# Kernel tuning notes

Hardware: AMD Instinct MI355X
Metric: run time of the kernel (lower is better)

Reference implementation:

```python
import jax, jax.numpy as jnp
import numpy as np

B, IN, H = 4096, 1024, 2048

def setup_inputs() -> dict:
    key = jax.random.key(0)
    ks = jax.random.split(key, 7)
    sk = (1.0 / H) ** 0.5
    return {
        "x": jax.random.normal(ks[0], (B, IN), dtype=jnp.float32),
        "prev_h": jax.random.normal(ks[1], (B, H), dtype=jnp.float32),
        "prev_c": jax.random.normal(ks[2], (B, H), dtype=jnp.float32),
        "W_i": jax.random.uniform(ks[3], (H, H + IN), dtype=jnp.float32, minval=-sk, maxval=sk),
        "W_f": jax.random.uniform(ks[4], (H, H + IN), dtype=jnp.float32, minval=-sk, maxval=sk),
        "W_o": jax.random.uniform(ks[5], (H, H + IN), dtype=jnp.float32, minval=-sk, maxval=sk),
        "W_c": jax.random.uniform(ks[6], (H, H + IN), dtype=jnp.float32, minval=-sk, maxval=sk),
    }

def reference(x, prev_h, prev_c, W_i, W_f, W_o, W_c):
    # concat (h, x) along features: [B, H+IN]
    hx = jnp.concatenate([prev_h, x], axis=1)
    # stack 4 gate weights -> single GEMM: [B, H+IN] @ [H+IN, 4H]
    W = jnp.concatenate([W_i, W_f, W_o, W_c], axis=0)  # [4H, H+IN]
    gates = hx @ W.T  # [B, 4H]
    gi, gf, go, gc = jnp.split(gates, 4, axis=1)
    i = jax.nn.sigmoid(gi)
    f = jax.nn.sigmoid(gf)
    o = jax.nn.sigmoid(go)
    c_tilde = jnp.tanh(gc)
    next_c = f * prev_c + i * c_tilde
    next_h = o * jnp.tanh(next_c)
    return next_h, next_c
```

## Files before the change

kernel.cpp:

```cpp
#include <hip/hip_runtime.h>
#include <hip/hip_bf16.h>


#define BATCH 4096
#define INW   1024
#define HID   2048
#define GK    3072
#define GN    8192

typedef __attribute__((ext_vector_type(8))) short short8;
typedef __attribute__((ext_vector_type(4))) float floatx4;

__device__ __forceinline__ unsigned short f2bf(float f) {
    union { float f; unsigned u; } v; v.f = f;
    unsigned r = v.u + 0x7FFFu + ((v.u >> 16) & 1u);
    return (unsigned short)(r >> 16);
}
__device__ __forceinline__ float sigf(float x) {
    return 1.0f / (1.0f + __expf(-x));
}
__device__ __forceinline__ float tanhfast(float x) {
    float t = __expf(fminf(fmaxf(2.0f * x, -30.0f), 30.0f));
    return (t - 1.0f) / (t + 1.0f);
}

__global__ __launch_bounds__(256) void pack_all(const float4* __restrict__ ph,
                                                const float4* __restrict__ x,
                                                const float4* __restrict__ Wi,
                                                const float4* __restrict__ Wf,
                                                const float4* __restrict__ Wo,
                                                const float4* __restrict__ Wc,
                                                unsigned short* __restrict__ hx,
                                                unsigned short* __restrict__ Wb) {
    long i = (long)blockIdx.x * 256 + threadIdx.x;
    const float4* src;
    unsigned short* dst;
    if (i < 1048576L) {
        int r  = (int)(i >> 8);
        int c8 = (int)(i & 255);
        src = ph + 2 * i;
        dst = hx + (size_t)r * GK + (size_t)c8 * 8;
    } else if (i < 1572864L) {
        long j = i - 1048576L;
        int r  = (int)(j >> 7);
        int c8 = (int)(j & 127);
        src = x + 2 * j;
        dst = hx + (size_t)r * GK + HID + (size_t)c8 * 8;
    } else {
        long j = i - 1572864L;
        const float4* Wg;
        int g;
        if (j < 786432L)            { Wg = Wi; g = 0; }
        else if (j < 1572864L)      { Wg = Wf; g = 1; j -= 786432L; }
        else if (j < 2359296L)      { Wg = Wo; g = 2; j -= 1572864L; }
        else                        { Wg = Wc; g = 3; j -= 2359296L; }
        src = Wg + 2 * j;
        int h  = (int)(j / 384);
        int kc = (int)(j - (long)h * 384);
        dst = Wb + (size_t)(4 * h + g) * GK + (size_t)kc * 8;
    }
    float4 v0 = src[0];
    float4 v1 = src[1];
    unsigned short o[8];
    o[0] = f2bf(v0.x); o[1] = f2bf(v0.y); o[2] = f2bf(v0.z); o[3] = f2bf(v0.w);
    o[4] = f2bf(v1.x); o[5] = f2bf(v1.y); o[6] = f2bf(v1.z); o[7] = f2bf(v1.w);
    *(short8*)dst = *(const short8*)o;
}

__device__ __forceinline__ void gld16(const unsigned short* g, unsigned short* l) {
    __builtin_amdgcn_global_load_lds((const __attribute__((address_space(1))) unsigned int*)g,
                                     (__attribute__((address_space(3))) unsigned int*)l,
                                     16, 0, 0);
}

template<int VM> __device__ __forceinline__ void wait_vm() {
    if constexpr (VM == 8)      asm volatile("s_waitcnt vmcnt(8)" ::: "memory");
    else if constexpr (VM == 4) asm volatile("s_waitcnt vmcnt(4)" ::: "memory");
    else if constexpr (VM == 0) asm volatile("s_waitcnt vmcnt(0)" ::: "memory");
}

__global__ __launch_bounds__(512, 2) void gemm_fused(const unsigned short* __restrict__ A,
                                                     const unsigned short* __restrict__ Bt,
                                                     const float* __restrict__ prev_c,
                                                     float* __restrict__ out) {
    __shared__ unsigned short lds[65536];
    const int tid  = threadIdx.x;
    const int wave = tid >> 6;
    const int lane = tid & 63;

    const int bid = blockIdx.x;
    const int x = bid & 7, ii = bid >> 3;
    const int mt = ((x & 3) << 2) + (ii & 3);
    const int nt = ((x >> 2) << 4) + (ii >> 2);
    const long row0 = (long)mt * 256;
    const long col0 = (long)nt * 256;

    const int wm = wave >> 2;
    const int wn = wave & 3;

    const int c0 = ((tid & 3) - ((tid >> 3) & 3)) & 3;
    const unsigned short* gA0 = A  + (row0 + (tid >> 2)) * GK + c0 * 8;
    const unsigned short* gB0 = Bt + (col0 + (tid >> 2)) * GK + c0 * 8;

#define STAGE_A(kt, b) do { \
        unsigned short* _d = &lds[(b) * 8192 + tid * 8]; \
        gld16(gA0 + (size_t)(kt) * 32, _d); \
        gld16(gA0 + 128 * GK + (size_t)(kt) * 32, _d + 4096); \
    } while (0)
#define STAGE_B(kt, b) do { \
        unsigned short* _d = &lds[32768 + (b) * 8192 + tid * 8]; \
        gld16(gB0 + (size_t)(kt) * 32, _d); \
        gld16(gB0 + 128 * GK + (size_t)(kt) * 32, _d + 4096); \
    } while (0)

    const int fr = lane & 15;
    const int cq = lane >> 4;
    const int slot = ((cq + (fr >> 1)) & 3) << 3;
    const int aoff = (wm * 128 + fr) * 32 + slot;
    const int boff = (wn * 64 + fr) * 32 + slot;

    floatx4 acc[8][4];
    #pragma unroll
    for (int i = 0; i < 8; i++)
        #pragma unroll
        for (int j = 0; j < 4; j++)
            acc[i][j] = (floatx4)(0.0f);

    STAGE_A(0, 0); STAGE_B(0, 0);
    STAGE_A(1, 1); STAGE_B(1, 1);
    STAGE_A(2, 2); STAGE_B(2, 2);
    asm volatile("s_waitcnt vmcnt(8)" ::: "memory");
    __builtin_amdgcn_s_barrier();

#define K_ITER(t, VMW, STG) do { \
        const unsigned short* bufA = &lds[((t) & 3) * 8192]; \
        const unsigned short* bufB = &lds[32768 + ((t) & 3) * 8192]; \
        short8 af[4], af2[4], bfv[4]; \
        _Pragma("unroll") \
        for (int i = 0; i < 4; i++) af[i]  = *(const short8*)&bufA[aoff + i * 512]; \
        _Pragma("unroll") \
        for (int j = 0; j < 4; j++) bfv[j] = *(const short8*)&bufB[boff + j * 512]; \
        __builtin_amdgcn_sched_barrier(0);  \
        _Pragma("unroll") \
        for (int i = 0; i < 4; i++) af2[i] = *(const short8*)&bufA[aoff + 2048 + i * 512]; \
        if (STG) { STAGE_A((t) + 3, ((t) + 3) & 3); STAGE_B((t) + 3, ((t) + 3) & 3); } \
        __builtin_amdgcn_s_barrier(); \
        asm volatile("s_waitcnt lgkmcnt(4)" ::: "memory"); \
        __builtin_amdgcn_sched_barrier(0); \
        __builtin_amdgcn_s_setprio(1); \
        _Pragma("unroll") \
        for (int i = 0; i < 4; i++) \
            _Pragma("unroll") \
            for (int j = 0; j < 4; j++) \
                acc[i][j] = __builtin_amdgcn_mfma_f32_16x16x32_bf16(af[i], bfv[j], acc[i][j], 0, 0, 0); \
        __builtin_amdgcn_s_setprio(0); \
        asm volatile("s_waitcnt lgkmcnt(0)" ::: "memory"); \
        __builtin_amdgcn_sched_barrier(0); \
        __builtin_amdgcn_s_setprio(1); \
        _Pragma("unroll") \
        for (int i = 0; i < 4; i++) \
            _Pragma("unroll") \
            for (int j = 0; j < 4; j++) \
                acc[4 + i][j] = __builtin_amdgcn_mfma_f32_16x16x32_bf16(af2[i], bfv[j], acc[4 + i][j], 0, 0, 0); \
        __builtin_amdgcn_s_setprio(0); \
        wait_vm<VMW>(); \
        __builtin_amdgcn_s_barrier(); \
    } while (0)

    int t = 0;
    for (; t < 93; ++t) K_ITER(t, 8, true);
    K_ITER(93, 4, false);
    K_ITER(94, 0, false);
    K_ITER(95, -1, false);

#undef K_ITER
#undef STAGE_A
#undef STAGE_B

    const int cr = (lane >> 4) << 2;
    const int cc = lane & 15;
    const int g  = lane & 3;
    float* nhl = (float*)lds;
    float* ncl = nhl + 16384;
    const long hbase = col0 >> 2;

    #pragma unroll
    for (int mi = 0; mi < 8; mi++) {
        #pragma unroll
        for (int nj = 0; nj < 4; nj++) {
            #pragma unroll
            for (int r = 0; r < 4; r++) {
                const int row_loc = wm * 128 + mi * 16 + cr + r;
                const int h_loc   = wn * 16 + nj * 4 + (cc >> 2);
                float v   = acc[mi][nj][r];
                float act = (g == 3) ? tanhfast(v) : sigf(v);
                float t1 = __shfl_xor(act, 1);
                float t2 = __shfl_xor(act, 2);
                float t3 = __shfl_xor(act, 3);
                float iv = (g == 0) ? act : (g == 1) ? t1 : (g == 2) ? t2 : t3;
                float fv = (g == 0) ? t1 : (g == 1) ? act : (g == 2) ? t3 : t2;
                float ov = (g == 0) ? t2 : (g == 1) ? t3 : (g == 2) ? act : t1;
                float cv = (g == 0) ? t3 : (g == 1) ? t2 : (g == 2) ? t1 : act;
                float pc = prev_c[(row0 + row_loc) * (long)HID + hbase + h_loc];
                float nc = fv * pc + iv * cv;
                float nh = ov * tanhfast(nc);
                if (g == 0)      nhl[row_loc * 64 + h_loc] = nh;
                else if (g == 1) ncl[row_loc * 64 + h_loc] = nc;
            }
        }
    }
    __syncthreads();

    #pragma unroll
    for (int p = 0; p < 8; p++) {
        const int idx = p * 512 + tid;
        const int row_loc = idx >> 4;
        const int h4 = (idx & 15) << 2;
        float4 vh = *(float4*)&nhl[row_loc * 64 + h4];
        float4 vc = *(float4*)&ncl[row_loc * 64 + h4];
        *(float4*)&out[(row0 + row_loc) * (long)HID + hbase + h4] = vh;
        *(float4*)&out[(size_t)BATCH * HID + (row0 + row_loc) * (long)HID + hbase + h4] = vc;
    }
}

extern "C" void kernel_launch(void* const* d_in, const int* in_sizes, int n_in,
                              void* d_out, int out_size, void* d_ws, size_t ws_size,
                              hipStream_t stream) {
    const float* x   = (const float*)d_in[0];
    const float* ph  = (const float*)d_in[1];
    const float* pc  = (const float*)d_in[2];
    const float* Wi  = (const float*)d_in[3];
    const float* Wf  = (const float*)d_in[4];
    const float* Wo  = (const float*)d_in[5];
    const float* Wc  = (const float*)d_in[6];

    unsigned short* hx = (unsigned short*)d_ws;
    unsigned short* Wb = hx + (size_t)BATCH * GK;
    float* out = (float*)d_out;

    pack_all<<<18432, 256, 0, stream>>>((const float4*)ph, (const float4*)x,
                                        (const float4*)Wi, (const float4*)Wf,
                                        (const float4*)Wo, (const float4*)Wc,
                                        hx, Wb);

    gemm_fused<<<512, 512, 0, stream>>>(hx, Wb, pc, out);
}
```

Before: 468.1 us.

## Move mid-iteration barrier and restage LSTM epilogue through LDS

The main loop's second barrier and the global-load wait move from the end of each iteration into the gap between the two MFMA halves, so the barrier overlaps with outstanding compute rather than serialising at the tail. The epilogue no longer shuffles gate values across lanes in registers. Instead the raw accumulators are staged into LDS in two passes, one per half of the warp rows, and each thread then reads a float4 of the four gates and computes the cell update with coalesced-ish prev_c reads. This removes redundant activation and shuffle work but adds extra LDS traffic, synchronisation passes, and scalar rather than float4 output stores.

```diff
diff --git a/kernel.cpp b/kernel.cpp
--- a/kernel.cpp
+++ b/kernel.cpp
@@ -144,7 +144,6 @@
         _Pragma("unroll") \
         for (int i = 0; i < 4; i++) af2[i] = *(const short8*)&bufA[aoff + 2048 + i * 512]; \
         if (STG) { STAGE_A((t) + 3, ((t) + 3) & 3); STAGE_B((t) + 3, ((t) + 3) & 3); } \
-        __builtin_amdgcn_s_barrier(); \
         asm volatile("s_waitcnt lgkmcnt(4)" ::: "memory"); \
         __builtin_amdgcn_sched_barrier(0); \
         __builtin_amdgcn_s_setprio(1); \
@@ -156,6 +155,9 @@
         __builtin_amdgcn_s_setprio(0); \
         asm volatile("s_waitcnt lgkmcnt(0)" ::: "memory"); \
         __builtin_amdgcn_sched_barrier(0); \
+        wait_vm<VMW>(); \
+        __builtin_amdgcn_s_barrier(); \
+        __builtin_amdgcn_sched_barrier(0); \
         __builtin_amdgcn_s_setprio(1); \
         _Pragma("unroll") \
         for (int i = 0; i < 4; i++) \
@@ -163,8 +165,6 @@
             for (int j = 0; j < 4; j++) \
                 acc[4 + i][j] = __builtin_amdgcn_mfma_f32_16x16x32_bf16(af2[i], bfv[j], acc[4 + i][j], 0, 0, 0); \
         __builtin_amdgcn_s_setprio(0); \
-        wait_vm<VMW>(); \
-        __builtin_amdgcn_s_barrier(); \
     } while (0)
 
     int t = 0;
@@ -179,47 +179,43 @@
 
     const int cr = (lane >> 4) << 2;
     const int cc = lane & 15;
-    const int g  = lane & 3;
-    float* nhl = (float*)lds;
-    float* ncl = nhl + 16384;
     const long hbase = col0 >> 2;
-
-    #pragma unroll
-    for (int mi = 0; mi < 8; mi++) {
-        #pragma unroll
-        for (int nj = 0; nj < 4; nj++) {
+    float* gbuf = (float*)lds;
+
+    #pragma unroll 1
+    for (int pass = 0; pass < 2; ++pass) {
+        __syncthreads();
+        if (wm == pass) {
             #pragma unroll
-            for (int r = 0; r < 4; r++) {
-                const int row_loc = wm * 128 + mi * 16 + cr + r;
-                const int h_loc   = wn * 16 + nj * 4 + (cc >> 2);
-                float v   = acc[mi][nj][r];
-                float act = (g == 3) ? tanhfast(v) : sigf(v);
-                float t1 = __shfl_xor(act, 1);
-                float t2 = __shfl_xor(act, 2);
-                float t3 = __shfl_xor(act, 3);
-                float iv = (g == 0) ? act : (g == 1) ? t1 : (g == 2) ? t2 : t3;
-                float fv = (g == 0) ? t1 : (g == 1) ? act : (g == 2) ? t3 : t2;
-                float ov = (g == 0) ? t2 : (g == 1) ? t3 : (g == 2) ? act : t1;
-                float cv = (g == 0) ? t3 : (g == 1) ? t2 : (g == 2) ? t1 : act;
-                float pc = prev_c[(row0 + row_loc) * (long)HID + hbase + h_loc];
-                float nc = fv * pc + iv * cv;
-                float nh = ov * tanhfast(nc);
-                if (g == 0)      nhl[row_loc * 64 + h_loc] = nh;
-                else if (g == 1) ncl[row_loc * 64 + h_loc] = nc;
+            for (int mi = 0; mi < 8; mi++) {
+                #pragma unroll
+                for (int nj = 0; nj < 4; nj++) {
+                    const int colb = wn * 64 + nj * 16 + cc;
+                    #pragma unroll
+                    for (int r = 0; r < 4; r++)
+                        gbuf[(mi * 16 + cr + r) * 256 + colb] = acc[mi][nj][r];
+                }
             }
         }
-    }
-    __syncthreads();
-
-    #pragma unroll
-    for (int p = 0; p < 8; p++) {
-        const int idx = p * 512 + tid;
-        const int row_loc = idx >> 4;
-        const int h4 = (idx & 15) << 2;
-        float4 vh = *(float4*)&nhl[row_loc * 64 + h4];
-        float4 vc = *(float4*)&ncl[row_loc * 64 + h4];
-        *(float4*)&out[(row0 + row_loc) * (long)HID + hbase + h4] = vh;
-        *(float4*)&out[(size_t)BATCH * HID + (row0 + row_loc) * (long)HID + hbase + h4] = vc;
+        __syncthreads();
+        #pragma unroll 4
+        for (int p = 0; p < 16; p++) {
+            const int u   = p * 512 + tid;
+            const int row = u >> 6;
+            const int h   = u & 63;
+            float4 g4 = *(const float4*)&gbuf[row * 256 + h * 4];
+            const long grow = row0 + pass * 128 + row;
+            const long ob   = grow * (long)HID + hbase + h;
+            float pc = prev_c[ob];
+            float iv = sigf(g4.x);
+            float fv = sigf(g4.y);
+            float ov = sigf(g4.z);
+            float cv = tanhfast(g4.w);
+            float nc = fv * pc + iv * cv;
+            float nh = ov * tanhfast(nc);
+            out[ob] = nh;
+            out[(size_t)BATCH * HID + ob] = nc;
+        }
     }
 }
 
```

Measured after the change: 402.2 us. 14.1% less time.
